# Optimization experiments

Hardware: AMD Instinct MI355X
Metric: run time of the kernel (lower is better)

The kernel has to match this reference:

```python
import jax, jax.numpy as jnp
import numpy as np

B, L, D, H, FF = 8, 512, 1024, 16, 1024
HD = D // H
EPS = 1e-5
ROPE_BASE = 10000.0
ROPE_DIM = D  # module passes dim=embed_dim (not head_dim) to RotaryPositionalEmbeddings


def _layer_norm(x, g, b):
    m = jnp.mean(x, axis=-1, keepdims=True)
    v = jnp.var(x, axis=-1, keepdims=True)
    return (x - m) * jax.lax.rsqrt(v + EPS) * g + b


def _rope(x):
    # x: [B, H, L, HD]; interleaved-pair rotation, frequencies base**(-2i/ROPE_DIM)
    half = HD // 2
    inv_freq = 1.0 / (ROPE_BASE ** (jnp.arange(half, dtype=jnp.float32) * 2.0 / ROPE_DIM))
    ang = jnp.arange(L, dtype=jnp.float32)[:, None] * inv_freq[None, :]  # [L, half]
    cos = jnp.cos(ang)
    sin = jnp.sin(ang)
    xr = x.reshape(*x.shape[:-1], half, 2)
    x1, x2 = xr[..., 0], xr[..., 1]
    out = jnp.stack([x1 * cos - x2 * sin, x1 * sin + x2 * cos], axis=-1)
    return out.reshape(x.shape).astype(x.dtype)


def setup_inputs() -> dict:
    key = jax.random.key(0)
    ks = jax.random.split(key, 16)
    sd = 0.02
    n = lambda k, shape: (jax.random.normal(k, shape, dtype=jnp.float32) * sd)
    return {
        "input_ids": jax.random.normal(ks[0], (B, L, D), dtype=jnp.float32),
        "Wq": n(ks[1], (FF, D)), "bq": jnp.zeros((D,), jnp.float32),
        "Wk": n(ks[2], (FF, D)), "bk": jnp.zeros((D,), jnp.float32),
        "Wv": n(ks[3], (FF, D)), "bv": jnp.zeros((D,), jnp.float32),
        "Wo": n(ks[4], (D, D)),  "bo": jnp.zeros((D,), jnp.float32),
        "Wf": n(ks[5], (D, FF)), "bf": jnp.zeros((FF,), jnp.float32),
        "g_ffn": jnp.ones((D,), jnp.float32), "b_ffn": jnp.zeros((D,), jnp.float32),
        "g_attn": jnp.ones((FF,), jnp.float32), "b_attn": jnp.zeros((FF,), jnp.float32),
    }


def reference(input_ids, Wq, bq, Wk, bk, Wv, bv, Wo, bo, Wf, bf,
              g_ffn, b_ffn, g_attn, b_attn):
    # FFN branch: computed then DISCARDED in the original source (x is overwritten).
    _ffn_dead = jax.nn.relu(_layer_norm(input_ids, g_ffn, b_ffn) @ Wf + bf)  # noqa: F841

    x = _layer_norm(input_ids, g_attn, b_attn)  # pre_attn_norm applied to input_ids
    q = (x @ Wq + bq).reshape(B, L, H, HD).transpose(0, 2, 1, 3)  # [B,H,L,HD]
    k = (x @ Wk + bk).reshape(B, L, H, HD).transpose(0, 2, 1, 3)
    v = (x @ Wv + bv).reshape(B, L, H, HD).transpose(0, 2, 1, 3)
    q = _rope(q)
    k = _rope(k)

    scale = 1.0 / np.sqrt(HD).astype(np.float32)
    scores = jnp.einsum("bhqd,bhkd->bhqk", q, k) * scale  # [B,H,L,L]
    attn = jax.nn.softmax(scores, axis=-1)
    o = jnp.einsum("bhqk,bhkd->bhqd", attn, v)
    o = o.transpose(0, 2, 1, 3).reshape(B, L, D)
    return input_ids + (o @ Wo + bo)
```

## Files before the change

kernel.cpp:

```cpp
#include <hip/hip_runtime.h>

typedef unsigned short ushort_t;
typedef short bf16x8 __attribute__((ext_vector_type(8)));
typedef float f32x4 __attribute__((ext_vector_type(4)));

#define B_ 8
#define L_ 512
#define D_ 1024
#define H_ 16
#define M_ 4096

__device__ __forceinline__ ushort_t f2bf(float f) {
  union { float f; unsigned u; } v; v.f = f;
  unsigned r = v.u + 0x7FFFu + ((v.u >> 16) & 1u);
  return (ushort_t)(r >> 16);
}

__device__ __forceinline__ void gl_lds16(const ushort_t* g, ushort_t* s) {
  __builtin_amdgcn_global_load_lds((const __attribute__((address_space(1))) void*)(g),
                                   (__attribute__((address_space(3))) void*)(s), 16, 0, 0);
}

__global__ __launch_bounds__(256) void prep_kernel(const float* __restrict__ x,
                                                   const float* __restrict__ g,
                                                   const float* __restrict__ b,
                                                   ushort_t* __restrict__ xn,
                                                   float2* __restrict__ csb,
                                                   const float* __restrict__ w0,
                                                   const float* __restrict__ w1,
                                                   const float* __restrict__ w2,
                                                   const float* __restrict__ w3,
                                                   ushort_t* __restrict__ wt) {
  __shared__ float tile[32][33];
  int blk = blockIdx.x, t = threadIdx.x;
  if (blk < 1024) {
    int row = blk * 4 + (t >> 6);
    int lane = t & 63;
    const float4* xr = (const float4*)(x + (size_t)row * D_);
    float4 v[4];
    float s = 0.f, s2 = 0.f;
#pragma unroll
    for (int j = 0; j < 4; ++j) {
      v[j] = xr[j * 64 + lane];
      s  += v[j].x + v[j].y + v[j].z + v[j].w;
      s2 += v[j].x * v[j].x + v[j].y * v[j].y + v[j].z * v[j].z + v[j].w * v[j].w;
    }
#pragma unroll
    for (int m = 1; m < 64; m <<= 1) { s += __shfl_xor(s, m); s2 += __shfl_xor(s2, m); }
    float mean = s * (1.0f / D_);
    float var  = s2 * (1.0f / D_) - mean * mean;
    float rs   = rsqrtf(var + 1e-5f);
    unsigned long long* outp = (unsigned long long*)(xn + (size_t)row * D_);
#pragma unroll
    for (int j = 0; j < 4; ++j) {
      float4 gg = ((const float4*)g)[j * 64 + lane];
      float4 bb = ((const float4*)b)[j * 64 + lane];
      unsigned long long pk =
          (unsigned long long)f2bf((v[j].x - mean) * rs * gg.x + bb.x)
        | ((unsigned long long)f2bf((v[j].y - mean) * rs * gg.y + bb.y) << 16)
        | ((unsigned long long)f2bf((v[j].z - mean) * rs * gg.z + bb.z) << 32)
        | ((unsigned long long)f2bf((v[j].w - mean) * rs * gg.w + bb.w) << 48);
      outp[j * 64 + lane] = pk;
    }
  } else if (blk < 1088) {
    int idx = (blk - 1024) * 256 + t;
    int l = idx >> 5, i = idx & 31;
    float inv = powf(10000.0f, (-2.0f * (float)i) / 1024.0f);
    float ang = (float)l * inv;
    csb[idx] = make_float2(cosf(ang), sinf(ang));
  } else {
    int wb = blk - 1088;
    int z = wb >> 10;
    const float* W = (z == 0) ? w0 : (z == 1) ? w1 : (z == 2) ? w2 : w3;
    ushort_t* WT = wt + ((size_t)z << 20);
    int rem = wb & 1023;
    int by = rem >> 5, bx = rem & 31;
    int tx = t & 31, ty = t >> 5;
    int k0 = by * 32, n0 = bx * 32;
#pragma unroll
    for (int j = 0; j < 4; ++j)
      tile[ty + 8 * j][tx] = W[(size_t)(k0 + ty + 8 * j) * 1024 + n0 + tx];
    __syncthreads();
#pragma unroll
    for (int j = 0; j < 4; ++j)
      WT[(size_t)(n0 + ty + 8 * j) * 1024 + k0 + tx] = f2bf(tile[tx][ty + 8 * j]);
  }
}

__global__ __launch_bounds__(128) void gemm_qkv_kernel(const ushort_t* __restrict__ xn,
                                                       const ushort_t* __restrict__ wt,
                                                       const float* __restrict__ bq,
                                                       const float* __restrict__ bk,
                                                       const float* __restrict__ bv,
                                                       ushort_t* __restrict__ qb,
                                                       ushort_t* __restrict__ kb,
                                                       ushort_t* __restrict__ vt,
                                                       const float2* __restrict__ csb) {
  __shared__ ushort_t As[64 * 64];
  __shared__ ushort_t Bs[64 * 64];
  int t = threadIdx.x, l = t & 63, w = t >> 6, lr = l & 15, lg = l >> 4;
  int hid = blockIdx.x;
  int xcd = hid & 7, lid = hid >> 3;
  int by = (xcd >> 1) * 16 + lid / 24;
  int bx = (xcd & 1) * 24 + lid % 24;
  int m0 = by * 64;
  int n0g = bx * 64;
  int z = n0g >> 10;
  int n0 = n0g & 1023;
  const float* bias = (z == 0) ? bq : (z == 1) ? bk : bv;
  const int sr8 = l >> 3;
  const int scol = ((l & 7) ^ sr8) * 8;

  f32x4 acc[2][4] = {};

  for (int k0 = 0; k0 < 1024; k0 += 64) {
#pragma unroll
    for (int i = 0; i < 4; ++i) {
      gl_lds16(&xn[(size_t)(m0 + w * 32 + i * 8 + sr8) * 1024 + k0 + scol],
               &As[(w * 32 + i * 8) * 64]);
      gl_lds16(&wt[(size_t)(n0g + w * 32 + i * 8 + sr8) * 1024 + k0 + scol],
               &Bs[(w * 32 + i * 8) * 64]);
    }
    __syncthreads();
#pragma unroll
    for (int kk = 0; kk < 2; ++kk) {
      bf16x8 a[2], bfr[4];
#pragma unroll
      for (int mi = 0; mi < 2; ++mi)
        a[mi] = *(const bf16x8*)&As[(w * 32 + mi * 16 + lr) * 64 + (((kk * 4 + lg) ^ (lr & 7)) << 3)];
#pragma unroll
      for (int ni = 0; ni < 4; ++ni)
        bfr[ni] = *(const bf16x8*)&Bs[(ni * 16 + lr) * 64 + (((kk * 4 + lg) ^ (lr & 7)) << 3)];
#pragma unroll
      for (int mi = 0; mi < 2; ++mi)
#pragma unroll
        for (int ni = 0; ni < 4; ++ni)
          acc[mi][ni] = __builtin_amdgcn_mfma_f32_16x16x32_bf16(a[mi], bfr[ni], acc[mi][ni], 0, 0, 0);
    }
    __syncthreads();
  }

  if (z < 2) {
    ushort_t* outp = (z == 0) ? qb : kb;
    const float sc = (z == 0) ? 0.125f : 1.0f;
#pragma unroll
    for (int mi = 0; mi < 2; ++mi) {
      int rowb = m0 + w * 32 + mi * 16 + lg * 4;
#pragma unroll
      for (int ni = 0; ni < 4; ++ni) {
        int col = n0 + ni * 16 + lr;
        float bvv = bias[col];
        int ii = (col & 63) >> 1;
        int codd = col & 1;
#pragma unroll
        for (int r = 0; r < 4; ++r) {
          float val = acc[mi][ni][r] + bvv;
          float par = __shfl_xor(val, 1);
          float2 cs = csb[((rowb + r) & 511) * 32 + ii];
          float y = codd ? (par * cs.y + val * cs.x) : (val * cs.x - par * cs.y);
          outp[(size_t)(rowb + r) * 1024 + col] = f2bf(y * sc);
        }
      }
    }
  } else {
#pragma unroll
    for (int mi = 0; mi < 2; ++mi) {
      int rowb = m0 + w * 32 + mi * 16 + lg * 4;
      int bidx = rowb >> 9, l0 = rowb & 511;
#pragma unroll
      for (int ni = 0; ni < 4; ++ni) {
        int col = n0 + ni * 16 + lr;
        float bvv = bias[col];
        unsigned long long pk =
            (unsigned long long)f2bf(acc[mi][ni][0] + bvv)
          | ((unsigned long long)f2bf(acc[mi][ni][1] + bvv) << 16)
          | ((unsigned long long)f2bf(acc[mi][ni][2] + bvv) << 32)
          | ((unsigned long long)f2bf(acc[mi][ni][3] + bvv) << 48);
        *(unsigned long long*)&vt[((size_t)(bidx << 10) + col) * 512 + l0] = pk;
      }
    }
  }
}

__global__ __launch_bounds__(256) void gemm_o_kernel(const ushort_t* __restrict__ A,
                                                     const ushort_t* __restrict__ Bt,
                                                     const float* __restrict__ bias,
                                                     const float* __restrict__ res,
                                                     float* __restrict__ out) {
  __shared__ ushort_t As[64 * 64];
  __shared__ ushort_t Bs[128 * 64];
  int t = threadIdx.x, l = t & 63, w = t >> 6, lr = l & 15, lg = l >> 4;
  int hid = blockIdx.x;
  int lid = (hid & 7) * 64 + (hid >> 3);
  int bx = lid & 7, by = lid >> 3;
  int m0 = by * 64, n0 = bx * 128;
  int wr = w >> 1, wc = w & 1;
  const int srow = l >> 3;
  const int scol = ((l & 7) ^ (srow & 7)) * 8;

  f32x4 acc[2][4] = {};

  for (int k0 = 0; k0 < 1024; k0 += 64) {
#pragma unroll
    for (int i = 0; i < 2; ++i)
      gl_lds16(&A[(size_t)(m0 + w * 16 + i * 8 + srow) * 1024 + k0 + scol],
               &As[(w * 16 + i * 8) * 64]);
#pragma unroll
    for (int i = 0; i < 4; ++i)
      gl_lds16(&Bt[(size_t)(n0 + w * 32 + i * 8 + srow) * 1024 + k0 + scol],
               &Bs[(w * 32 + i * 8) * 64]);
    __syncthreads();
#pragma unroll
    for (int kk = 0; kk < 2; ++kk) {
      bf16x8 a[2], bfr[4];
#pragma unroll
      for (int mi = 0; mi < 2; ++mi)
        a[mi] = *(const bf16x8*)&As[(wr * 32 + mi * 16 + lr) * 64 + (((kk * 4 + lg) ^ (lr & 7)) << 3)];
#pragma unroll
      for (int ni = 0; ni < 4; ++ni)
        bfr[ni] = *(const bf16x8*)&Bs[(wc * 64 + ni * 16 + lr) * 64 + (((kk * 4 + lg) ^ (lr & 7)) << 3)];
#pragma unroll
      for (int mi = 0; mi < 2; ++mi)
#pragma unroll
        for (int ni = 0; ni < 4; ++ni)
          acc[mi][ni] = __builtin_amdgcn_mfma_f32_16x16x32_bf16(a[mi], bfr[ni], acc[mi][ni], 0, 0, 0);
    }
    __syncthreads();
  }

#pragma unroll
  for (int mi = 0; mi < 2; ++mi) {
    int rowb = m0 + wr * 32 + mi * 16 + lg * 4;
#pragma unroll
    for (int ni = 0; ni < 4; ++ni) {
      int col = n0 + wc * 64 + ni * 16 + lr;
      float bvv = bias[col];
#pragma unroll
      for (int r = 0; r < 4; ++r) {
        size_t off = (size_t)(rowb + r) * 1024 + col;
        out[off] = acc[mi][ni][r] + bvv + res[off];
      }
    }
  }
}

__global__ __launch_bounds__(256) void attn_kernel(const ushort_t* __restrict__ q,
                                                   const ushort_t* __restrict__ k,
                                                   const ushort_t* __restrict__ vt,
                                                   ushort_t* __restrict__ o) {
  __shared__ ushort_t Ks[2][64 * 64];
  __shared__ ushort_t Vs[2][64 * 64];
  __shared__ ushort_t Ps[4][2][16 * 64];
  int t = threadIdx.x, l = t & 63, w = t >> 6, lr = l & 15, lg = l >> 4;
  int blk = blockIdx.x;
  int bh = blk & 127, qt = blk >> 7;
  int b = bh >> 4, h = bh & 15;
  const int srow = l >> 3;
  const int scol = ((l & 7) ^ (srow & 7)) * 8;

  bf16x8 qf[2][2];
#pragma unroll
  for (int qm = 0; qm < 2; ++qm) {
    size_t qrow = (size_t)(b * 512 + qt * 128 + w * 32 + qm * 16 + lr);
#pragma unroll
    for (int kh = 0; kh < 2; ++kh)
      qf[qm][kh] = *(const bf16x8*)&q[qrow * 1024 + h * 64 + kh * 32 + lg * 8];
  }

  f32x4 oacc[2][4] = {};
  float mrun[2] = {-1e30f, -1e30f};
  float lrun[2] = {0.f, 0.f};

#define STAGE(buf, kv0)                                                              \
  {                                                                                  \
    _Pragma("unroll")                                                                \
    for (int j = 0; j < 2; ++j) {                                                    \
      gl_lds16(&k[(size_t)(b * 512 + (kv0) + w * 16 + j * 8 + srow) * 1024 + h * 64 + scol], \
               &Ks[buf][(w * 16 + j * 8) * 64]);                                     \
      gl_lds16(&vt[((size_t)bh * 64 + w * 16 + j * 8 + srow) * 512 + (kv0) + scol],  \
               &Vs[buf][(w * 16 + j * 8) * 64]);                                     \
    }                                                                                \
  }

  STAGE(0, 0);
  __syncthreads();
  int cur = 0;
  for (int it = 0; it < 8; ++it) {
    if (it < 7) { STAGE(cur ^ 1, (it + 1) * 64); }
    bf16x8 kf[2][4];
#pragma unroll
    for (int kh = 0; kh < 2; ++kh)
#pragma unroll
      for (int kn = 0; kn < 4; ++kn)
        kf[kh][kn] = *(const bf16x8*)&Ks[cur][(kn * 16 + lr) * 64 + (((kh * 4 + lg) ^ (lr & 7)) << 3)];

#pragma unroll
    for (int qm = 0; qm < 2; ++qm) {
      f32x4 st[4] = {};
#pragma unroll
      for (int kh = 0; kh < 2; ++kh)
#pragma unroll
        for (int kn = 0; kn < 4; ++kn)
          st[kn] = __builtin_amdgcn_mfma_f32_16x16x32_bf16(kf[kh][kn], qf[qm][kh], st[kn], 0, 0, 0);
      float mx = st[0][0];
#pragma unroll
      for (int kn = 0; kn < 4; ++kn)
#pragma unroll
        for (int r = 0; r < 4; ++r) mx = fmaxf(mx, st[kn][r]);
      mx = fmaxf(mx, __shfl_xor(mx, 16));
      mx = fmaxf(mx, __shfl_xor(mx, 32));
      float mn = mrun[qm], al = 1.0f;
      if (!__all(mx <= mrun[qm] + 8.0f)) {
        mn = fmaxf(mrun[qm], mx);
        al = __expf(mrun[qm] - mn);
        mrun[qm] = mn;
#pragma unroll
        for (int f = 0; f < 4; ++f) {
          oacc[qm][f][0] *= al; oacc[qm][f][1] *= al;
          oacc[qm][f][2] *= al; oacc[qm][f][3] *= al;
        }
      }
      float sm = 0.f;
#pragma unroll
      for (int kn = 0; kn < 4; ++kn) {
        float p0 = __expf(st[kn][0] - mn);
        float p1 = __expf(st[kn][1] - mn);
        float p2 = __expf(st[kn][2] - mn);
        float p3 = __expf(st[kn][3] - mn);
        sm += p0 + p1 + p2 + p3;
        int kvb = kn * 16 + 4 * lg;
        unsigned long long pk =
            (unsigned long long)f2bf(p0)
          | ((unsigned long long)f2bf(p1) << 16)
          | ((unsigned long long)f2bf(p2) << 32)
          | ((unsigned long long)f2bf(p3) << 48);
        *(unsigned long long*)&Ps[w][qm][lr * 64 + (((kvb >> 3) ^ (lr & 7)) << 3) + (kvb & 7)] = pk;
      }
      sm += __shfl_xor(sm, 16);
      sm += __shfl_xor(sm, 32);
      lrun[qm] = lrun[qm] * al + sm;
    }
    asm volatile("s_waitcnt lgkmcnt(0)" ::: "memory");
    __builtin_amdgcn_sched_barrier(0);
#pragma unroll
    for (int kk = 0; kk < 2; ++kk) {
      int sl = (((kk * 4 + lg) ^ (lr & 7)) << 3);
      bf16x8 pb[2];
#pragma unroll
      for (int qm = 0; qm < 2; ++qm)
        pb[qm] = *(const bf16x8*)&Ps[w][qm][lr * 64 + sl];
#pragma unroll
      for (int f = 0; f < 4; ++f) {
        bf16x8 vf = *(const bf16x8*)&Vs[cur][(f * 16 + lr) * 64 + sl];
#pragma unroll
        for (int qm = 0; qm < 2; ++qm)
          oacc[qm][f] = __builtin_amdgcn_mfma_f32_16x16x32_bf16(vf, pb[qm], oacc[qm][f], 0, 0, 0);
      }
    }
    __syncthreads();
    cur ^= 1;
  }
#pragma unroll
  for (int qm = 0; qm < 2; ++qm) {
    float inv = 1.0f / lrun[qm];
    size_t qrow = (size_t)(b * 512 + qt * 128 + w * 32 + qm * 16 + lr);
#pragma unroll
    for (int f = 0; f < 4; ++f) {
      unsigned long long pk =
          (unsigned long long)f2bf(oacc[qm][f][0] * inv)
        | ((unsigned long long)f2bf(oacc[qm][f][1] * inv) << 16)
        | ((unsigned long long)f2bf(oacc[qm][f][2] * inv) << 32)
        | ((unsigned long long)f2bf(oacc[qm][f][3] * inv) << 48);
      *(unsigned long long*)&o[qrow * 1024 + h * 64 + f * 16 + 4 * lg] = pk;
    }
  }
#undef STAGE
}

extern "C" void kernel_launch(void* const* d_in, const int* in_sizes, int n_in,
                              void* d_out, int out_size, void* d_ws, size_t ws_size,
                              hipStream_t stream) {
  const float* input_ids = (const float*)d_in[0];
  const float* Wq = (const float*)d_in[1];
  const float* bq = (const float*)d_in[2];
  const float* Wk = (const float*)d_in[3];
  const float* bk = (const float*)d_in[4];
  const float* Wv = (const float*)d_in[5];
  const float* bv = (const float*)d_in[6];
  const float* Wo = (const float*)d_in[7];
  const float* bo = (const float*)d_in[8];
  const float* g_attn = (const float*)d_in[13];
  const float* b_attn = (const float*)d_in[14];
  float* out = (float*)d_out;

  char* ws = (char*)d_ws;
  const size_t MB = 1024 * 1024;
  ushort_t* wt = (ushort_t*)(ws);
  ushort_t* xn = (ushort_t*)(ws + 8 * MB);
  ushort_t* qb = (ushort_t*)(ws + 16 * MB);
  ushort_t* kb = (ushort_t*)(ws + 24 * MB);
  ushort_t* vt = (ushort_t*)(ws + 32 * MB);
  float2* csb  = (float2*)(ws + 40 * MB);

  prep_kernel<<<5184, 256, 0, stream>>>(input_ids, g_attn, b_attn, xn, csb,
                                        Wq, Wk, Wv, Wo, wt);
  gemm_qkv_kernel<<<3072, 128, 0, stream>>>(xn, wt, bq, bk, bv, qb, kb, vt, csb);
  attn_kernel<<<512, 256, 0, stream>>>(qb, kb, vt, xn);
  gemm_o_kernel<<<512, 256, 0, stream>>>(xn, wt + 3 * MB, bo, input_ids, out);
}
```

Baseline: 93.45 us.

## Retile QKV, attention and output-projection kernels for different block/wave granularity

The QKV GEMM moves to 64x128 tiles with four waves in a 2x2 arrangement, halving its grid. The attention kernel drops from 32 to 16 query rows per wave, doubling the grid to 1024 blocks. The output projection switches to single-wave 32x64 tiles across 2048 blocks with an XCD-aware mapping. The aim is to rebalance occupancy and CU fill across the three kernels. In exchange, attention loses K-fragment reuse across two query tiles, and the small O-GEMM tiles reload the shared operands more often.

```diff
diff --git a/kernel.cpp b/kernel.cpp
--- a/kernel.cpp
+++ b/kernel.cpp
@@ -87,7 +87,7 @@
   }
 }
 
-__global__ __launch_bounds__(128) void gemm_qkv_kernel(const ushort_t* __restrict__ xn,
+__global__ __launch_bounds__(256) void gemm_qkv_kernel(const ushort_t* __restrict__ xn,
                                                        const ushort_t* __restrict__ wt,
                                                        const float* __restrict__ bq,
                                                        const float* __restrict__ bk,
@@ -97,40 +97,40 @@
                                                        ushort_t* __restrict__ vt,
                                                        const float2* __restrict__ csb) {
   __shared__ ushort_t As[64 * 64];
-  __shared__ ushort_t Bs[64 * 64];
+  __shared__ ushort_t Bs[128 * 64];
   int t = threadIdx.x, l = t & 63, w = t >> 6, lr = l & 15, lg = l >> 4;
   int hid = blockIdx.x;
   int xcd = hid & 7, lid = hid >> 3;
-  int by = (xcd >> 1) * 16 + lid / 24;
-  int bx = (xcd & 1) * 24 + lid % 24;
+  int by = (xcd >> 1) * 16 + lid / 12;
+  int bx = (xcd & 1) * 12 + lid % 12;
   int m0 = by * 64;
-  int n0g = bx * 64;
+  int n0g = bx * 128;
   int z = n0g >> 10;
   int n0 = n0g & 1023;
   const float* bias = (z == 0) ? bq : (z == 1) ? bk : bv;
+  int wr = w >> 1, wc = w & 1;
   const int sr8 = l >> 3;
   const int scol = ((l & 7) ^ sr8) * 8;
 
   f32x4 acc[2][4] = {};
 
   for (int k0 = 0; k0 < 1024; k0 += 64) {
-#pragma unroll
-    for (int i = 0; i < 4; ++i) {
-      gl_lds16(&xn[(size_t)(m0 + w * 32 + i * 8 + sr8) * 1024 + k0 + scol],
-               &As[(w * 32 + i * 8) * 64]);
-      gl_lds16(&wt[(size_t)(n0g + w * 32 + i * 8 + sr8) * 1024 + k0 + scol],
-               &Bs[(w * 32 + i * 8) * 64]);
-    }
+    gl_lds16(&xn[(size_t)(m0 + w * 16 + sr8) * 1024 + k0 + scol], &As[(w * 16) * 64]);
+    gl_lds16(&xn[(size_t)(m0 + w * 16 + 8 + sr8) * 1024 + k0 + scol], &As[(w * 16 + 8) * 64]);
+    gl_lds16(&wt[(size_t)(n0g + w * 32 + sr8) * 1024 + k0 + scol], &Bs[(w * 32) * 64]);
+    gl_lds16(&wt[(size_t)(n0g + w * 32 + 8 + sr8) * 1024 + k0 + scol], &Bs[(w * 32 + 8) * 64]);
+    gl_lds16(&wt[(size_t)(n0g + w * 32 + 16 + sr8) * 1024 + k0 + scol], &Bs[(w * 32 + 16) * 64]);
+    gl_lds16(&wt[(size_t)(n0g + w * 32 + 24 + sr8) * 1024 + k0 + scol], &Bs[(w * 32 + 24) * 64]);
     __syncthreads();
 #pragma unroll
     for (int kk = 0; kk < 2; ++kk) {
       bf16x8 a[2], bfr[4];
 #pragma unroll
       for (int mi = 0; mi < 2; ++mi)
-        a[mi] = *(const bf16x8*)&As[(w * 32 + mi * 16 + lr) * 64 + (((kk * 4 + lg) ^ (lr & 7)) << 3)];
+        a[mi] = *(const bf16x8*)&As[(wr * 32 + mi * 16 + lr) * 64 + (((kk * 4 + lg) ^ (lr & 7)) << 3)];
 #pragma unroll
       for (int ni = 0; ni < 4; ++ni)
-        bfr[ni] = *(const bf16x8*)&Bs[(ni * 16 + lr) * 64 + (((kk * 4 + lg) ^ (lr & 7)) << 3)];
+        bfr[ni] = *(const bf16x8*)&Bs[(wc * 64 + ni * 16 + lr) * 64 + (((kk * 4 + lg) ^ (lr & 7)) << 3)];
 #pragma unroll
       for (int mi = 0; mi < 2; ++mi)
 #pragma unroll
@@ -145,10 +145,10 @@
     const float sc = (z == 0) ? 0.125f : 1.0f;
 #pragma unroll
     for (int mi = 0; mi < 2; ++mi) {
-      int rowb = m0 + w * 32 + mi * 16 + lg * 4;
+      int rowb = m0 + wr * 32 + mi * 16 + lg * 4;
 #pragma unroll
       for (int ni = 0; ni < 4; ++ni) {
-        int col = n0 + ni * 16 + lr;
+        int col = n0 + wc * 64 + ni * 16 + lr;
         float bvv = bias[col];
         int ii = (col & 63) >> 1;
         int codd = col & 1;
@@ -165,11 +165,11 @@
   } else {
 #pragma unroll
     for (int mi = 0; mi < 2; ++mi) {
-      int rowb = m0 + w * 32 + mi * 16 + lg * 4;
+      int rowb = m0 + wr * 32 + mi * 16 + lg * 4;
       int bidx = rowb >> 9, l0 = rowb & 511;
 #pragma unroll
       for (int ni = 0; ni < 4; ++ni) {
-        int col = n0 + ni * 16 + lr;
+        int col = n0 + wc * 64 + ni * 16 + lr;
         float bvv = bias[col];
         unsigned long long pk =
             (unsigned long long)f2bf(acc[mi][ni][0] + bvv)
@@ -182,43 +182,41 @@
   }
 }
 
-__global__ __launch_bounds__(256) void gemm_o_kernel(const ushort_t* __restrict__ A,
-                                                     const ushort_t* __restrict__ Bt,
-                                                     const float* __restrict__ bias,
-                                                     const float* __restrict__ res,
-                                                     float* __restrict__ out) {
-  __shared__ ushort_t As[64 * 64];
-  __shared__ ushort_t Bs[128 * 64];
-  int t = threadIdx.x, l = t & 63, w = t >> 6, lr = l & 15, lg = l >> 4;
+__global__ __launch_bounds__(64) void gemm_o_kernel(const ushort_t* __restrict__ A,
+                                                    const ushort_t* __restrict__ Bt,
+                                                    const float* __restrict__ bias,
+                                                    const float* __restrict__ res,
+                                                    float* __restrict__ out) {
+  __shared__ ushort_t As[32 * 64];
+  __shared__ ushort_t Bs[64 * 64];
+  int l = threadIdx.x, lr = l & 15, lg = l >> 4;
   int hid = blockIdx.x;
-  int lid = (hid & 7) * 64 + (hid >> 3);
-  int bx = lid & 7, by = lid >> 3;
-  int m0 = by * 64, n0 = bx * 128;
-  int wr = w >> 1, wc = w & 1;
-  const int srow = l >> 3;
-  const int scol = ((l & 7) ^ (srow & 7)) * 8;
+  int xcd = hid & 7, lid = hid >> 3;
+  int by = xcd * 16 + (lid >> 4);
+  int bx = lid & 15;
+  int m0 = by * 32, n0 = bx * 64;
+  const int sr8 = l >> 3;
+  const int scol = ((l & 7) ^ sr8) * 8;
 
   f32x4 acc[2][4] = {};
 
   for (int k0 = 0; k0 < 1024; k0 += 64) {
 #pragma unroll
-    for (int i = 0; i < 2; ++i)
-      gl_lds16(&A[(size_t)(m0 + w * 16 + i * 8 + srow) * 1024 + k0 + scol],
-               &As[(w * 16 + i * 8) * 64]);
-#pragma unroll
     for (int i = 0; i < 4; ++i)
-      gl_lds16(&Bt[(size_t)(n0 + w * 32 + i * 8 + srow) * 1024 + k0 + scol],
-               &Bs[(w * 32 + i * 8) * 64]);
+      gl_lds16(&A[(size_t)(m0 + i * 8 + sr8) * 1024 + k0 + scol], &As[(i * 8) * 64]);
+#pragma unroll
+    for (int i = 0; i < 8; ++i)
+      gl_lds16(&Bt[(size_t)(n0 + i * 8 + sr8) * 1024 + k0 + scol], &Bs[(i * 8) * 64]);
     __syncthreads();
 #pragma unroll
     for (int kk = 0; kk < 2; ++kk) {
       bf16x8 a[2], bfr[4];
 #pragma unroll
       for (int mi = 0; mi < 2; ++mi)
-        a[mi] = *(const bf16x8*)&As[(wr * 32 + mi * 16 + lr) * 64 + (((kk * 4 + lg) ^ (lr & 7)) << 3)];
+        a[mi] = *(const bf16x8*)&As[(mi * 16 + lr) * 64 + (((kk * 4 + lg) ^ (lr & 7)) << 3)];
 #pragma unroll
       for (int ni = 0; ni < 4; ++ni)
-        bfr[ni] = *(const bf16x8*)&Bs[(wc * 64 + ni * 16 + lr) * 64 + (((kk * 4 + lg) ^ (lr & 7)) << 3)];
+        bfr[ni] = *(const bf16x8*)&Bs[(ni * 16 + lr) * 64 + (((kk * 4 + lg) ^ (lr & 7)) << 3)];
 #pragma unroll
       for (int mi = 0; mi < 2; ++mi)
 #pragma unroll
@@ -230,10 +228,10 @@
 
 #pragma unroll
   for (int mi = 0; mi < 2; ++mi) {
-    int rowb = m0 + wr * 32 + mi * 16 + lg * 4;
+    int rowb = m0 + mi * 16 + lg * 4;
 #pragma unroll
     for (int ni = 0; ni < 4; ++ni) {
-      int col = n0 + wc * 64 + ni * 16 + lr;
+      int col = n0 + ni * 16 + lr;
       float bvv = bias[col];
 #pragma unroll
       for (int r = 0; r < 4; ++r) {
@@ -250,7 +248,7 @@
                                                    ushort_t* __restrict__ o) {
   __shared__ ushort_t Ks[2][64 * 64];
   __shared__ ushort_t Vs[2][64 * 64];
-  __shared__ ushort_t Ps[4][2][16 * 64];
+  __shared__ ushort_t Ps[4][16 * 64];
   int t = threadIdx.x, l = t & 63, w = t >> 6, lr = l & 15, lg = l >> 4;
   int blk = blockIdx.x;
   int bh = blk & 127, qt = blk >> 7;
@@ -258,18 +256,17 @@
   const int srow = l >> 3;
   const int scol = ((l & 7) ^ (srow & 7)) * 8;
 
-  bf16x8 qf[2][2];
-#pragma unroll
-  for (int qm = 0; qm < 2; ++qm) {
-    size_t qrow = (size_t)(b * 512 + qt * 128 + w * 32 + qm * 16 + lr);
+  bf16x8 qf[2];
+  {
+    size_t qrow = (size_t)(b * 512 + qt * 64 + w * 16 + lr);
 #pragma unroll
     for (int kh = 0; kh < 2; ++kh)
-      qf[qm][kh] = *(const bf16x8*)&q[qrow * 1024 + h * 64 + kh * 32 + lg * 8];
-  }
-
-  f32x4 oacc[2][4] = {};
-  float mrun[2] = {-1e30f, -1e30f};
-  float lrun[2] = {0.f, 0.f};
+      qf[kh] = *(const bf16x8*)&q[qrow * 1024 + h * 64 + kh * 32 + lg * 8];
+  }
+
+  f32x4 oacc[4] = {};
+  float mrun = -1e30f;
+  float lrun = 0.f;
 
 #define STAGE(buf, kv0)                                                              \
   {                                                                                  \
@@ -287,90 +284,77 @@
   int cur = 0;
   for (int it = 0; it < 8; ++it) {
     if (it < 7) { STAGE(cur ^ 1, (it + 1) * 64); }
-    bf16x8 kf[2][4];
+    f32x4 st[4] = {};
 #pragma unroll
     for (int kh = 0; kh < 2; ++kh)
 #pragma unroll
-      for (int kn = 0; kn < 4; ++kn)
-        kf[kh][kn] = *(const bf16x8*)&Ks[cur][(kn * 16 + lr) * 64 + (((kh * 4 + lg) ^ (lr & 7)) << 3)];
-
-#pragma unroll
-    for (int qm = 0; qm < 2; ++qm) {
-      f32x4 st[4] = {};
-#pragma unroll
-      for (int kh = 0; kh < 2; ++kh)
-#pragma unroll
-        for (int kn = 0; kn < 4; ++kn)
-          st[kn] = __builtin_amdgcn_mfma_f32_16x16x32_bf16(kf[kh][kn], qf[qm][kh], st[kn], 0, 0, 0);
-      float mx = st[0][0];
-#pragma unroll
-      for (int kn = 0; kn < 4; ++kn)
-#pragma unroll
-        for (int r = 0; r < 4; ++r) mx = fmaxf(mx, st[kn][r]);
-      mx = fmaxf(mx, __shfl_xor(mx, 16));
-      mx = fmaxf(mx, __shfl_xor(mx, 32));
-      float mn = mrun[qm], al = 1.0f;
-      if (!__all(mx <= mrun[qm] + 8.0f)) {
-        mn = fmaxf(mrun[qm], mx);
-        al = __expf(mrun[qm] - mn);
-        mrun[qm] = mn;
-#pragma unroll
-        for (int f = 0; f < 4; ++f) {
-          oacc[qm][f][0] *= al; oacc[qm][f][1] *= al;
-          oacc[qm][f][2] *= al; oacc[qm][f][3] *= al;
-        }
-      }
-      float sm = 0.f;
-#pragma unroll
       for (int kn = 0; kn < 4; ++kn) {
-        float p0 = __expf(st[kn][0] - mn);
-        float p1 = __expf(st[kn][1] - mn);
-        float p2 = __expf(st[kn][2] - mn);
-        float p3 = __expf(st[kn][3] - mn);
-        sm += p0 + p1 + p2 + p3;
-        int kvb = kn * 16 + 4 * lg;
-        unsigned long long pk =
-            (unsigned long long)f2bf(p0)
-          | ((unsigned long long)f2bf(p1) << 16)
-          | ((unsigned long long)f2bf(p2) << 32)
-          | ((unsigned long long)f2bf(p3) << 48);
-        *(unsigned long long*)&Ps[w][qm][lr * 64 + (((kvb >> 3) ^ (lr & 7)) << 3) + (kvb & 7)] = pk;
-      }
-      sm += __shfl_xor(sm, 16);
-      sm += __shfl_xor(sm, 32);
-      lrun[qm] = lrun[qm] * al + sm;
-    }
+        bf16x8 kf = *(const bf16x8*)&Ks[cur][(kn * 16 + lr) * 64 + (((kh * 4 + lg) ^ (lr & 7)) << 3)];
+        st[kn] = __builtin_amdgcn_mfma_f32_16x16x32_bf16(kf, qf[kh], st[kn], 0, 0, 0);
+      }
+    float mx = st[0][0];
+#pragma unroll
+    for (int kn = 0; kn < 4; ++kn)
+#pragma unroll
+      for (int r = 0; r < 4; ++r) mx = fmaxf(mx, st[kn][r]);
+    mx = fmaxf(mx, __shfl_xor(mx, 16));
+    mx = fmaxf(mx, __shfl_xor(mx, 32));
+    float mn = mrun, al = 1.0f;
+    if (!__all(mx <= mrun + 8.0f)) {
+      mn = fmaxf(mrun, mx);
+      al = __expf(mrun - mn);
+      mrun = mn;
+#pragma unroll
+      for (int f = 0; f < 4; ++f) {
+        oacc[f][0] *= al; oacc[f][1] *= al;
+        oacc[f][2] *= al; oacc[f][3] *= al;
+      }
+    }
+    float sm = 0.f;
+#pragma unroll
+    for (int kn = 0; kn < 4; ++kn) {
+      float p0 = __expf(st[kn][0] - mn);
+      float p1 = __expf(st[kn][1] - mn);
+      float p2 = __expf(st[kn][2] - mn);
+      float p3 = __expf(st[kn][3] - mn);
+      sm += p0 + p1 + p2 + p3;
+      int kvb = kn * 16 + 4 * lg;
+      unsigned long long pk =
+          (unsigned long long)f2bf(p0)
+        | ((unsigned long long)f2bf(p1) << 16)
+        | ((unsigned long long)f2bf(p2) << 32)
+        | ((unsigned long long)f2bf(p3) << 48);
+      *(unsigned long long*)&Ps[w][lr * 64 + (((kvb >> 3) ^ (lr & 7)) << 3) + (kvb & 7)] = pk;
+    }
+    sm += __shfl_xor(sm, 16);
+    sm += __shfl_xor(sm, 32);
+    lrun = lrun * al + sm;
+
     asm volatile("s_waitcnt lgkmcnt(0)" ::: "memory");
     __builtin_amdgcn_sched_barrier(0);
 #pragma unroll
     for (int kk = 0; kk < 2; ++kk) {
       int sl = (((kk * 4 + lg) ^ (lr & 7)) << 3);
-      bf16x8 pb[2];
-#pragma unroll
-      for (int qm = 0; qm < 2; ++qm)
-        pb[qm] = *(const bf16x8*)&Ps[w][qm][lr * 64 + sl];
+      bf16x8 pb = *(const bf16x8*)&Ps[w][lr * 64 + sl];
 #pragma unroll
       for (int f = 0; f < 4; ++f) {
         bf16x8 vf = *(const bf16x8*)&Vs[cur][(f * 16 + lr) * 64 + sl];
-#pragma unroll
-        for (int qm = 0; qm < 2; ++qm)
-          oacc[qm][f] = __builtin_amdgcn_mfma_f32_16x16x32_bf16(vf, pb[qm], oacc[qm][f], 0, 0, 0);
+        oacc[f] = __builtin_amdgcn_mfma_f32_16x16x32_bf16(vf, pb, oacc[f], 0, 0, 0);
       }
     }
     __syncthreads();
     cur ^= 1;
   }
-#pragma unroll
-  for (int qm = 0; qm < 2; ++qm) {
-    float inv = 1.0f / lrun[qm];
-    size_t qrow = (size_t)(b * 512 + qt * 128 + w * 32 + qm * 16 + lr);
+  {
+    float inv = 1.0f / lrun;
+    size_t qrow = (size_t)(b * 512 + qt * 64 + w * 16 + lr);
 #pragma unroll
     for (int f = 0; f < 4; ++f) {
       unsigned long long pk =
-          (unsigned long long)f2bf(oacc[qm][f][0] * inv)
-        | ((unsigned long long)f2bf(oacc[qm][f][1] * inv) << 16)
-        | ((unsigned long long)f2bf(oacc[qm][f][2] * inv) << 32)
-        | ((unsigned long long)f2bf(oacc[qm][f][3] * inv) << 48);
+          (unsigned long long)f2bf(oacc[f][0] * inv)
+        | ((unsigned long long)f2bf(oacc[f][1] * inv) << 16)
+        | ((unsigned long long)f2bf(oacc[f][2] * inv) << 32)
+        | ((unsigned long long)f2bf(oacc[f][3] * inv) << 48);
       *(unsigned long long*)&o[qrow * 1024 + h * 64 + f * 16 + 4 * lg] = pk;
     }
   }
@@ -404,7 +388,7 @@
 
   prep_kernel<<<5184, 256, 0, stream>>>(input_ids, g_attn, b_attn, xn, csb,
                                         Wq, Wk, Wv, Wo, wt);
-  gemm_qkv_kernel<<<3072, 128, 0, stream>>>(xn, wt, bq, bk, bv, qb, kb, vt, csb);
-  attn_kernel<<<512, 256, 0, stream>>>(qb, kb, vt, xn);
-  gemm_o_kernel<<<512, 256, 0, stream>>>(xn, wt + 3 * MB, bo, input_ids, out);
-}
+  gemm_qkv_kernel<<<1536, 256, 0, stream>>>(xn, wt, bq, bk, bv, qb, kb, vt, csb);
+  attn_kernel<<<1024, 256, 0, stream>>>(qb, kb, vt, xn);
+  gemm_o_kernel<<<2048, 64, 0, stream>>>(xn, wt + 3 * MB, bo, input_ids, out);
+}
```

Result: faster. 90.86 us (-2.8%).
